# Optimization experiments

Measured on AMD Instinct MI355X. Metric: run time of the kernel, lower is better.

The kernel has to match this reference:

```python
import jax, jax.numpy as jnp
import numpy as np

P = 256          # planes == in_planes
EPS = 1e-5       # BatchNorm eps


def binarize(x):
    # sign with sign(0) -> +1, as in standard binary-net quantizers
    return jnp.where(x >= 0, 1.0, -1.0).astype(x.dtype)


def bin_conv(x, w, stride=1):
    """XNOR-style binarized 3x3 conv: sign(x) * sign(w), scaled by per-out-channel mean |w|."""
    ba = binarize(x)
    bw = binarize(w)
    scale = jnp.mean(jnp.abs(w), axis=(1, 2, 3))  # [O]
    y = jax.lax.conv_general_dilated(
        ba, bw, window_strides=(stride, stride), padding=((1, 1), (1, 1)),
        dimension_numbers=("NCHW", "OIHW", "NCHW"))
    return y * scale[None, :, None, None]


def bn(x, gamma, beta, mean, var):
    # inference-mode BatchNorm2d
    inv = gamma / jnp.sqrt(var + EPS)
    return x * inv[None, :, None, None] + (beta - mean * inv)[None, :, None, None]


def channel_shuffle(x, groups=2):
    b, c, h, w = x.shape
    return x.reshape(b, groups, c // groups, h, w).transpose(0, 2, 1, 3, 4).reshape(b, c, h, w)


def setup_inputs() -> dict:
    key = jax.random.key(0)
    ks = jax.random.split(key, 8)
    B, H, W = 16, 56, 56
    return {
        "x": jax.random.normal(ks[0], (B, 2 * P, H, W), jnp.float32),
        "w1": jax.random.normal(ks[1], (P, P, 3, 3), jnp.float32) * 0.05,
        "w2": jax.random.normal(ks[2], (P, 2 * P, 3, 3), jnp.float32) * 0.05,
        "gamma1": jnp.ones((P,), jnp.float32),
        "beta1": jnp.zeros((P,), jnp.float32),
        "mean1": jax.random.normal(ks[3], (P,), jnp.float32) * 0.1,
        "var1": jax.random.uniform(ks[4], (P,), jnp.float32) + 0.5,
        "gamma2": jnp.ones((P,), jnp.float32),
        "beta2": jnp.zeros((P,), jnp.float32),
        "mean2": jax.random.normal(ks[5], (P,), jnp.float32) * 0.1,
        "var2": jax.random.uniform(ks[6], (P,), jnp.float32) + 0.5,
        "move_bias": jax.random.normal(ks[7], (1, P, 1, 1), jnp.float32) * 0.1,
    }


def reference(x, w1, w2, gamma1, beta1, mean1, var1,
              gamma2, beta2, mean2, var2, move_bias):
    x_act, x_idle = x[:, :P], x[:, P:]
    residual = x_act
    out = bn(bin_conv(x_act, w1, stride=1), gamma1, beta1, mean1, var1)
    out = out + residual
    out = jnp.clip(out, -1.0, 1.0)            # Hardtanh
    x_idle = x_idle + move_bias               # LearnableBias
    out = jnp.concatenate([out, x_idle], axis=1)   # [B, 2P, H, W]
    out = channel_shuffle(out, groups=2)
    residual1 = out[:, :P]
    out = bn(bin_conv(out, w2, stride=1), gamma2, beta2, mean2, var2)
    out = out + residual1
    out = jnp.clip(out, -1.0, 1.0)            # Hardtanh
    return out
```

## Files before the change

### kernel.cpp

```cpp
#include <hip/hip_runtime.h>
#include <cstdint>

typedef unsigned long long u64;

#define HWSZ 3136
#define WD 56
#define NPIX 50176
#define NB 16

__device__ __forceinline__ float clampf(float v){ return fminf(1.0f, fmaxf(-1.0f, v)); }

__global__ __launch_bounds__(256) void k_wprep(
    const float* __restrict__ w1, const float* __restrict__ w2,
    const float* __restrict__ g1, const float* __restrict__ be1,
    const float* __restrict__ m1, const float* __restrict__ v1,
    const float* __restrict__ g2, const float* __restrict__ be2,
    const float* __restrict__ m2, const float* __restrict__ v2,
    u64* __restrict__ w1b, u64* __restrict__ w2e, u64* __restrict__ w2o,
    float* __restrict__ A1, float* __restrict__ B1,
    float* __restrict__ A2, float* __restrict__ B2)
{
    int co  = blockIdx.x;
    int tid = threadIdx.x;
    int wv = tid >> 6, lane = tid & 63;
    int ci = (wv << 6) + lane;

    float s1 = 0.f, s2 = 0.f;
    const float* w1p = w1 + ((size_t)co * 256 + ci) * 9;
#pragma unroll
    for (int t = 0; t < 9; t++) {
        float v = w1p[t];
        s1 += fabsf(v);
        u64 bal = __ballot(v >= 0.f);
        if (lane == 0) w1b[(co * 9 + t) * 4 + wv] = bal;
    }
    const float* wep = w2 + ((size_t)co * 512 + 2 * ci) * 9;
    const float* wop = wep + 9;
#pragma unroll
    for (int t = 0; t < 9; t++) {
        float ve = wep[t], vo = wop[t];
        s2 += fabsf(ve) + fabsf(vo);
        u64 bale = __ballot(ve >= 0.f);
        u64 balo = __ballot(vo >= 0.f);
        if (lane == 0) { w2e[(co * 9 + t) * 4 + wv] = bale; w2o[(co * 9 + t) * 4 + wv] = balo; }
    }
    __shared__ float red1[256], red2[256];
    red1[tid] = s1; red2[tid] = s2;
    __syncthreads();
    for (int off = 128; off > 0; off >>= 1) {
        if (tid < off) { red1[tid] += red1[tid + off]; red2[tid] += red2[tid + off]; }
        __syncthreads();
    }
    if (tid == 0) {
        float scale1 = red1[0] / 2304.f;
        float scale2 = red2[0] / 4608.f;
        float inv1 = g1[co] / sqrtf(v1[co] + 1e-5f);
        float inv2 = g2[co] / sqrtf(v2[co] + 1e-5f);
        A1[co] = scale1 * inv1;  B1[co] = be1[co] - m1[co] * inv1;
        A2[co] = scale2 * inv2;  B2[co] = be2[co] - m2[co] * inv2;
    }
}

__global__ __launch_bounds__(256) void k_pack(
    const float* __restrict__ x, const float* __restrict__ mb,
    u64* __restrict__ bitsA, u64* __restrict__ bitsI)
{
    int tid = threadIdx.x;
    int p = blockIdx.x * 256 + tid;
    int q = blockIdx.y;
    int b = p / HWSZ, hw = p % HWSZ;
    const float* xa = x + ((size_t)(b * 512 + q * 64)) * HWSZ + hw;
    const float* xi = x + ((size_t)(b * 512 + 256 + q * 64)) * HWSZ + hw;
    const float* mbq = mb + q * 64;
    u64 wa = 0, wi = 0;
#pragma unroll 8
    for (int j = 0; j < 64; j++) {
        float va = xa[(size_t)j * HWSZ];
        float vi = xi[(size_t)j * HWSZ] + mbq[j];
        wa |= (u64)(va >= 0.f) << j;
        wi |= (u64)(vi >= 0.f) << j;
    }
    bitsA[(size_t)p * 4 + q] = wa;
    bitsI[(size_t)p * 4 + q] = wi;
}

__global__ __launch_bounds__(256) void k_conv1(
    const float* __restrict__ x, const u64* __restrict__ bitsA,
    const u64* __restrict__ w1b, const float* __restrict__ A1, const float* __restrict__ B1,
    u64* __restrict__ bitsC, float* __restrict__ c1v)
{
    __shared__ u64 sw[2304];
    __shared__ float sA[64], sB[64];
    int tid = threadIdx.x;
    int q = blockIdx.y;
    int cobase = q * 64;
    {
        const u64* src = w1b + (size_t)cobase * 36;
#pragma unroll
        for (int i = 0; i < 9; i++) sw[tid + i * 256] = src[tid + i * 256];
        if (tid < 64) { sA[tid] = A1[cobase + tid]; sB[tid] = B1[cobase + tid]; }
    }
    __syncthreads();

    int p = blockIdx.x * 256 + tid;
    int b = p / HWSZ, hw = p % HWSZ;
    int h = hw / WD, w = hw % WD;

    int acc[64];
#pragma unroll
    for (int i = 0; i < 64; i++) acc[i] = 0;
    int nvalid = 0;
#pragma unroll 1
    for (int t = 0; t < 9; t++) {
        int dy = t / 3 - 1, dx = t % 3 - 1;
        int hh = h + dy, ww = w + dx;
        bool valid = (hh >= 0 && hh < WD && ww >= 0 && ww < WD);
        u64 n0 = 0, n1 = 0, n2 = 0, n3 = 0;
        if (valid) {
            const u64* nb = bitsA + (size_t)(p + dy * WD + dx) * 4;
            n0 = nb[0]; n1 = nb[1]; n2 = nb[2]; n3 = nb[3];
        }
        int mask = valid ? -1 : 0;
        nvalid -= mask;
#pragma unroll
        for (int co = 0; co < 64; co++) {
            const u64* wp = &sw[(co * 9 + t) * 4];
            int pt = __popcll(n0 ^ wp[0]) + __popcll(n1 ^ wp[1])
                   + __popcll(n2 ^ wp[2]) + __popcll(n3 ^ wp[3]);
            acc[co] += pt & mask;
        }
    }
    u64 signw = 0;
    const float* xr = x + ((size_t)(b * 512 + cobase)) * HWSZ + hw;
    float* cv = c1v + (size_t)cobase * NPIX + p;
#pragma unroll
    for (int co = 0; co < 64; co++) {
        int y = (nvalid << 8) - 2 * acc[co];
        float v = (float)y * sA[co] + sB[co] + xr[(size_t)co * HWSZ];
        signw |= (u64)(v >= 0.f) << co;
        if (q < 2) cv[(size_t)co * NPIX] = clampf(v);
    }
    bitsC[(size_t)p * 4 + q] = signw;
}

__global__ __launch_bounds__(256) void k_conv2(
    const float* __restrict__ x, const float* __restrict__ mb,
    const u64* __restrict__ bitsC, const u64* __restrict__ bitsI,
    const u64* __restrict__ w2e, const u64* __restrict__ w2o,
    const float* __restrict__ A2, const float* __restrict__ B2,
    const float* __restrict__ c1v, float* __restrict__ out)
{
    __shared__ u64 se[2304], so[2304];
    __shared__ float sA[64], sB[64], sM[32];
    int tid = threadIdx.x;
    int q = blockIdx.y;
    int cobase = q * 64;
    {
        const u64* srcE = w2e + (size_t)cobase * 36;
        const u64* srcO = w2o + (size_t)cobase * 36;
#pragma unroll
        for (int i = 0; i < 9; i++) { se[tid + i * 256] = srcE[tid + i * 256]; so[tid + i * 256] = srcO[tid + i * 256]; }
        if (tid < 64) { sA[tid] = A2[cobase + tid]; sB[tid] = B2[cobase + tid]; }
        if (tid < 32) { sM[tid] = mb[cobase / 2 + tid]; }
    }
    __syncthreads();

    int p = blockIdx.x * 256 + tid;
    int b = p / HWSZ, hw = p % HWSZ;
    int h = hw / WD, w = hw % WD;

    int acc[64];
#pragma unroll
    for (int i = 0; i < 64; i++) acc[i] = 0;
    int nvalid = 0;
#pragma unroll 1
    for (int t = 0; t < 9; t++) {
        int dy = t / 3 - 1, dx = t % 3 - 1;
        int hh = h + dy, ww = w + dx;
        bool valid = (hh >= 0 && hh < WD && ww >= 0 && ww < WD);
        u64 c0 = 0, c1 = 0, c2 = 0, c3 = 0, i0 = 0, i1 = 0, i2 = 0, i3 = 0;
        if (valid) {
            size_t np = (size_t)(p + dy * WD + dx) * 4;
            c0 = bitsC[np]; c1 = bitsC[np + 1]; c2 = bitsC[np + 2]; c3 = bitsC[np + 3];
            i0 = bitsI[np]; i1 = bitsI[np + 1]; i2 = bitsI[np + 2]; i3 = bitsI[np + 3];
        }
        int mask = valid ? -1 : 0;
        nvalid -= mask;
#pragma unroll
        for (int co = 0; co < 64; co++) {
            const u64* we = &se[(co * 9 + t) * 4];
            const u64* wo = &so[(co * 9 + t) * 4];
            int pt = __popcll(c0 ^ we[0]) + __popcll(c1 ^ we[1])
                   + __popcll(c2 ^ we[2]) + __popcll(c3 ^ we[3])
                   + __popcll(i0 ^ wo[0]) + __popcll(i1 ^ wo[1])
                   + __popcll(i2 ^ wo[2]) + __popcll(i3 ^ wo[3]);
            acc[co] += pt & mask;
        }
    }
    const float* xo = x + ((size_t)(b * 512 + 256 + 32 * q)) * HWSZ + hw;
    const float* cvr = c1v + (size_t)(32 * q) * NPIX + p;
    float* op = out + ((size_t)(b * 256 + cobase)) * HWSZ + hw;
#pragma unroll
    for (int co = 0; co < 64; co++) {
        int y = (nvalid << 9) - 2 * acc[co];
        float v = (float)y * sA[co] + sB[co];
        int cg2 = co >> 1;
        float res;
        if ((co & 1) == 0) res = cvr[(size_t)cg2 * NPIX];
        else               res = xo[(size_t)cg2 * HWSZ] + sM[cg2];
        v += res;
        op[(size_t)co * HWSZ] = clampf(v);
    }
}

extern "C" void kernel_launch(void* const* d_in, const int* in_sizes, int n_in,
                              void* d_out, int out_size, void* d_ws, size_t ws_size,
                              hipStream_t stream)
{
    const float* x   = (const float*)d_in[0];
    const float* w1  = (const float*)d_in[1];
    const float* w2  = (const float*)d_in[2];
    const float* g1  = (const float*)d_in[3];
    const float* be1 = (const float*)d_in[4];
    const float* m1  = (const float*)d_in[5];
    const float* v1  = (const float*)d_in[6];
    const float* g2  = (const float*)d_in[7];
    const float* be2 = (const float*)d_in[8];
    const float* m2  = (const float*)d_in[9];
    const float* v2  = (const float*)d_in[10];
    const float* mb  = (const float*)d_in[11];

    char* ws = (char*)d_ws;
    u64* w1b = (u64*)ws; ws += 73728;
    u64* w2e = (u64*)ws; ws += 73728;
    u64* w2o = (u64*)ws; ws += 73728;
    float* A1 = (float*)ws; ws += 1024;
    float* B1 = (float*)ws; ws += 1024;
    float* A2 = (float*)ws; ws += 1024;
    float* B2 = (float*)ws; ws += 1024;
    u64* bitsA = (u64*)ws; ws += (size_t)NPIX * 4 * 8;
    u64* bitsI = (u64*)ws; ws += (size_t)NPIX * 4 * 8;
    u64* bitsC = (u64*)ws; ws += (size_t)NPIX * 4 * 8;
    float* c1v = (float*)ws; ws += (size_t)128 * NPIX * 4;

    hipLaunchKernelGGL(k_wprep, dim3(256), dim3(256), 0, stream,
                       w1, w2, g1, be1, m1, v1, g2, be2, m2, v2,
                       w1b, w2e, w2o, A1, B1, A2, B2);
    hipLaunchKernelGGL(k_pack, dim3(196, 4), dim3(256), 0, stream, x, mb, bitsA, bitsI);
    hipLaunchKernelGGL(k_conv1, dim3(196, 4), dim3(256), 0, stream,
                       x, bitsA, w1b, A1, B1, bitsC, c1v);
    hipLaunchKernelGGL(k_conv2, dim3(196, 4), dim3(256), 0, stream,
                       x, mb, bitsC, bitsI, w2e, w2o, A2, B2, c1v, (float*)d_out);
}
```

Measured before the change: 462.0 us.

## Restructure binary convs with padded bit layout, per-thread pixel pairs, wave channel groups

The packed activation bits now live in a zero-padded 58x58 layout, so the conv inner loops drop per-tap validity masks. The popcount of padded zero bits is corrected through per-channel border sums precomputed in weight prep. Each thread now computes two adjacent pixels over 16 output channels, with waves splitting the 64-channel group. A row of neighbour bits is loaded once and reused across the three horizontal taps, and weights are read as wave-uniform scalars instead of from LDS in conv1. The intermediate clamp values are stored as bf16 to halve their traffic, and wider vector loads and stores are used. The cost is an extra zeroing kernel, more complex border correction logic, and bf16 rounding of the residual.

Result: slower. 484.1 us (+4.8%).

```diff
diff --git a/kernel.cpp b/kernel.cpp
--- a/kernel.cpp
+++ b/kernel.cpp
@@ -2,13 +2,67 @@
 #include <cstdint>
 
 typedef unsigned long long u64;
+typedef unsigned short u16;
 
 #define HWSZ 3136
 #define WD 56
 #define NPIX 50176
-#define NB 16
+#define HS 58
+#define IMG 3364
 
 __device__ __forceinline__ float clampf(float v){ return fminf(1.0f, fmaxf(-1.0f, v)); }
+__device__ __forceinline__ u16 f2bf(float f){
+    unsigned u = __float_as_uint(f);
+    return (u16)((u + 0x7fffu + ((u >> 16) & 1u)) >> 16);
+}
+__device__ __forceinline__ float bf2f(u16 h){ return __uint_as_float(((unsigned)h) << 16); }
+__device__ __forceinline__ int xp(u64 a, u64 b, int s){
+    u64 x = a ^ b;
+    s += __popc((unsigned)x);
+    s += __popc((unsigned)(x >> 32));
+    return s;
+}
+
+__device__ __forceinline__ void conv_pass(
+    const u64* __restrict__ bits, const u64* __restrict__ wsrc, int colbase,
+    int base, int (&accA)[8][2], int (&accB)[8][2])
+{
+#pragma unroll 1
+    for (int dy = -1; dy <= 1; dy++) {
+        const ulonglong2* rp = (const ulonglong2*)(bits + (size_t)(base + dy * HS) * 4);
+        ulonglong2 plo[4], phi[4];
+#pragma unroll
+        for (int k = 0; k < 4; k++) { plo[k] = rp[2 * k]; phi[k] = rp[2 * k + 1]; }
+        int tb = (dy + 1) * 3;
+#pragma unroll
+        for (int dx = 0; dx < 3; dx++) {
+#pragma unroll
+            for (int co = 0; co < 8; co++) {
+                const u64* wp = wsrc + ((size_t)(colbase + co) * 9 + tb + dx) * 4;
+                u64 wa0 = wp[0], wa1 = wp[1], wb0 = wp[2], wb1 = wp[3];
+#pragma unroll
+                for (int p = 0; p < 2; p++) {
+                    int k = dx + p; int s = accA[co][p];
+                    s = xp(plo[k].x, wa0, s); s = xp(plo[k].y, wa1, s);
+                    s = xp(phi[k].x, wb0, s); s = xp(phi[k].y, wb1, s);
+                    accA[co][p] = s;
+                }
+            }
+#pragma unroll
+            for (int co = 0; co < 8; co++) {
+                const u64* wp = wsrc + ((size_t)(colbase + 8 + co) * 9 + tb + dx) * 4;
+                u64 wa0 = wp[0], wa1 = wp[1], wb0 = wp[2], wb1 = wp[3];
+#pragma unroll
+                for (int p = 0; p < 2; p++) {
+                    int k = dx + p; int s = accB[co][p];
+                    s = xp(plo[k].x, wa0, s); s = xp(plo[k].y, wa1, s);
+                    s = xp(phi[k].x, wb0, s); s = xp(phi[k].y, wb1, s);
+                    accB[co][p] = s;
+                }
+            }
+        }
+    }
+}
 
 __global__ __launch_bounds__(256) void k_wprep(
     const float* __restrict__ w1, const float* __restrict__ w2,
@@ -18,13 +72,16 @@
     const float* __restrict__ m2, const float* __restrict__ v2,
     u64* __restrict__ w1b, u64* __restrict__ w2e, u64* __restrict__ w2o,
     float* __restrict__ A1, float* __restrict__ B1,
-    float* __restrict__ A2, float* __restrict__ B2)
+    float* __restrict__ A2, float* __restrict__ B2,
+    int* __restrict__ C1s, int* __restrict__ C2s)
 {
     int co  = blockIdx.x;
     int tid = threadIdx.x;
     int wv = tid >> 6, lane = tid & 63;
     int ci = (wv << 6) + lane;
 
+    __shared__ int spc1[4][9], spc2[4][9];
+
     float s1 = 0.f, s2 = 0.f;
     const float* w1p = w1 + ((size_t)co * 256 + ci) * 9;
 #pragma unroll
@@ -32,7 +89,7 @@
         float v = w1p[t];
         s1 += fabsf(v);
         u64 bal = __ballot(v >= 0.f);
-        if (lane == 0) w1b[(co * 9 + t) * 4 + wv] = bal;
+        if (lane == 0) { w1b[(co * 9 + t) * 4 + wv] = bal; spc1[wv][t] = __popcll(bal); }
     }
     const float* wep = w2 + ((size_t)co * 512 + 2 * ci) * 9;
     const float* wop = wep + 9;
@@ -42,7 +99,10 @@
         s2 += fabsf(ve) + fabsf(vo);
         u64 bale = __ballot(ve >= 0.f);
         u64 balo = __ballot(vo >= 0.f);
-        if (lane == 0) { w2e[(co * 9 + t) * 4 + wv] = bale; w2o[(co * 9 + t) * 4 + wv] = balo; }
+        if (lane == 0) {
+            w2e[(co * 9 + t) * 4 + wv] = bale; w2o[(co * 9 + t) * 4 + wv] = balo;
+            spc2[wv][t] = __popcll(bale) + __popcll(balo);
+        }
     }
     __shared__ float red1[256], red2[256];
     red1[tid] = s1; red2[tid] = s2;
@@ -58,7 +118,31 @@
         float inv2 = g2[co] / sqrtf(v2[co] + 1e-5f);
         A1[co] = scale1 * inv1;  B1[co] = be1[co] - m1[co] * inv1;
         A2[co] = scale2 * inv2;  B2[co] = be2[co] - m2[co] * inv2;
-    }
+        int pc1[9], pc2[9];
+#pragma unroll
+        for (int t = 0; t < 9; t++) {
+            pc1[t] = spc1[0][t] + spc1[1][t] + spc1[2][t] + spc1[3][t];
+            pc2[t] = spc2[0][t] + spc2[1][t] + spc2[2][t] + spc2[3][t];
+        }
+        int* c1 = C1s + co * 8;
+        c1[0] = pc1[0] + pc1[1] + pc1[2];
+        c1[1] = pc1[6] + pc1[7] + pc1[8];
+        c1[2] = pc1[0] + pc1[3] + pc1[6];
+        c1[3] = pc1[2] + pc1[5] + pc1[8];
+        c1[4] = pc1[0]; c1[5] = pc1[2]; c1[6] = pc1[6]; c1[7] = pc1[8];
+        int* c2 = C2s + co * 8;
+        c2[0] = pc2[0] + pc2[1] + pc2[2];
+        c2[1] = pc2[6] + pc2[7] + pc2[8];
+        c2[2] = pc2[0] + pc2[3] + pc2[6];
+        c2[3] = pc2[2] + pc2[5] + pc2[8];
+        c2[4] = pc2[0]; c2[5] = pc2[2]; c2[6] = pc2[6]; c2[7] = pc2[8];
+    }
+}
+
+__global__ __launch_bounds__(256) void k_zero(ulonglong2* __restrict__ dst, int n)
+{
+    int i = blockIdx.x * 256 + threadIdx.x;
+    if (i < n) { ulonglong2 z; z.x = 0; z.y = 0; dst[i] = z; }
 }
 
 __global__ __launch_bounds__(256) void k_pack(
@@ -69,6 +153,7 @@
     int p = blockIdx.x * 256 + tid;
     int q = blockIdx.y;
     int b = p / HWSZ, hw = p % HWSZ;
+    int h = hw / WD, w = hw % WD;
     const float* xa = x + ((size_t)(b * 512 + q * 64)) * HWSZ + hw;
     const float* xi = x + ((size_t)(b * 512 + 256 + q * 64)) * HWSZ + hw;
     const float* mbq = mb + q * 64;
@@ -80,136 +165,143 @@
         wa |= (u64)(va >= 0.f) << j;
         wi |= (u64)(vi >= 0.f) << j;
     }
-    bitsA[(size_t)p * 4 + q] = wa;
-    bitsI[(size_t)p * 4 + q] = wi;
-}
-
-__global__ __launch_bounds__(256) void k_conv1(
+    size_t pos = ((size_t)b * IMG + (h + 1) * HS + (w + 1)) * 4 + q;
+    bitsA[pos] = wa;
+    bitsI[pos] = wi;
+}
+
+__global__ __launch_bounds__(512, 6) void k_conv1(
     const float* __restrict__ x, const u64* __restrict__ bitsA,
-    const u64* __restrict__ w1b, const float* __restrict__ A1, const float* __restrict__ B1,
-    u64* __restrict__ bitsC, float* __restrict__ c1v)
-{
-    __shared__ u64 sw[2304];
+    const u64* __restrict__ w1b, const float* __restrict__ A1,
+    const float* __restrict__ B1, const int* __restrict__ C1s,
+    u64* __restrict__ bitsC, u16* __restrict__ c1v)
+{
     __shared__ float sA[64], sB[64];
-    int tid = threadIdx.x;
-    int q = blockIdx.y;
-    int cobase = q * 64;
-    {
-        const u64* src = w1b + (size_t)cobase * 36;
-#pragma unroll
-        for (int i = 0; i < 9; i++) sw[tid + i * 256] = src[tid + i * 256];
-        if (tid < 64) { sA[tid] = A1[cobase + tid]; sB[tid] = B1[cobase + tid]; }
-    }
+    __shared__ int scr[512];
+    __shared__ u16 spart[4][256];
+    int tid = threadIdx.x, q = blockIdx.y, cobase = q * 64;
+    if (tid < 64) { sA[tid] = A1[cobase + tid]; sB[tid] = B1[cobase + tid]; }
+    scr[tid] = C1s[cobase * 8 + tid];
     __syncthreads();
 
-    int p = blockIdx.x * 256 + tid;
-    int b = p / HWSZ, hw = p % HWSZ;
-    int h = hw / WD, w = hw % WD;
-
-    int acc[64];
-#pragma unroll
-    for (int i = 0; i < 64; i++) acc[i] = 0;
-    int nvalid = 0;
-#pragma unroll 1
-    for (int t = 0; t < 9; t++) {
-        int dy = t / 3 - 1, dx = t % 3 - 1;
-        int hh = h + dy, ww = w + dx;
-        bool valid = (hh >= 0 && hh < WD && ww >= 0 && ww < WD);
-        u64 n0 = 0, n1 = 0, n2 = 0, n3 = 0;
-        if (valid) {
-            const u64* nb = bitsA + (size_t)(p + dy * WD + dx) * 4;
-            n0 = nb[0]; n1 = nb[1]; n2 = nb[2]; n3 = nb[3];
-        }
-        int mask = valid ? -1 : 0;
-        nvalid -= mask;
-#pragma unroll
-        for (int co = 0; co < 64; co++) {
-            const u64* wp = &sw[(co * 9 + t) * 4];
-            int pt = __popcll(n0 ^ wp[0]) + __popcll(n1 ^ wp[1])
-                   + __popcll(n2 ^ wp[2]) + __popcll(n3 ^ wp[3]);
-            acc[co] += pt & mask;
-        }
-    }
-    u64 signw = 0;
-    const float* xr = x + ((size_t)(b * 512 + cobase)) * HWSZ + hw;
-    float* cv = c1v + (size_t)cobase * NPIX + p;
-#pragma unroll
-    for (int co = 0; co < 64; co++) {
-        int y = (nvalid << 8) - 2 * acc[co];
-        float v = (float)y * sA[co] + sB[co] + xr[(size_t)co * HWSZ];
-        signw |= (u64)(v >= 0.f) << co;
-        if (q < 2) cv[(size_t)co * NPIX] = clampf(v);
-    }
-    bitsC[(size_t)p * 4 + q] = signw;
-}
-
-__global__ __launch_bounds__(256) void k_conv2(
+    int wid = tid >> 6, lane = tid & 63;
+    int gu = __builtin_amdgcn_readfirstlane(wid & 3);
+    int ph = wid >> 2;
+    int pix0 = blockIdx.x * 256 + ph * 128 + lane * 2;
+    int b = pix0 / HWSZ, hw = pix0 % HWSZ, h = hw / WD, w = hw % WD;
+    int base = b * IMG + (h + 1) * HS + w;
+
+    int accA[8][2] = {}, accB[8][2] = {};
+    conv_pass(bitsA, w1b, cobase + (gu << 4), base, accA, accB);
+
+    int mt = (h == 0), mbo = (h == WD - 1);
+    int wl = (w == 0), wr = (w == 54);
+    int nvr = 3 - mt - mbo;
+    int nv0 = nvr * (3 - wl), nv1 = nvr * (3 - wr);
+
+    unsigned sb0 = 0, sb1 = 0;
+    bool wrv = (q < 2);
+#pragma unroll
+    for (int half = 0; half < 2; half++)
+#pragma unroll
+    for (int co = 0; co < 8; co++) {
+        int col = (gu << 4) + half * 8 + co;
+        int coG = cobase + col, bit = half * 8 + co;
+        float A = sA[col], Bc = sB[col];
+        const int* cs = &scr[col * 8];
+        int a0 = half ? accB[co][0] : accA[co][0];
+        int a1 = half ? accB[co][1] : accA[co][1];
+        int ctb = (mt ? cs[0] : 0) + (mbo ? cs[1] : 0);
+        int corr0 = ctb + (wl ? (cs[2] - (mt ? cs[4] : 0) - (mbo ? cs[6] : 0)) : 0);
+        int corr1 = ctb + (wr ? (cs[3] - (mt ? cs[5] : 0) - (mbo ? cs[7] : 0)) : 0);
+        float2 xr = *(const float2*)(x + ((size_t)(b * 512 + coG)) * HWSZ + hw);
+        float v0 = (float)((nv0 << 8) + 2 * (corr0 - a0)) * A + Bc + xr.x;
+        float v1 = (float)((nv1 << 8) + 2 * (corr1 - a1)) * A + Bc + xr.y;
+        sb0 |= (unsigned)(v0 >= 0.f) << bit;
+        sb1 |= (unsigned)(v1 >= 0.f) << bit;
+        if (wrv) {
+            ushort2 st; st.x = f2bf(clampf(v0)); st.y = f2bf(clampf(v1));
+            *(ushort2*)(c1v + (size_t)coG * NPIX + pix0) = st;
+        }
+    }
+    spart[gu][ph * 128 + lane * 2]     = (u16)sb0;
+    spart[gu][ph * 128 + lane * 2 + 1] = (u16)sb1;
+    __syncthreads();
+    if ((wid & 3) == 0) {
+#pragma unroll
+        for (int p = 0; p < 2; p++) {
+            int pi = ph * 128 + lane * 2 + p;
+            u64 word = (u64)spart[0][pi] | ((u64)spart[1][pi] << 16)
+                     | ((u64)spart[2][pi] << 32) | ((u64)spart[3][pi] << 48);
+            bitsC[(size_t)(base + 1 + p) * 4 + q] = word;
+        }
+    }
+}
+
+__global__ __launch_bounds__(512, 6) void k_conv2(
     const float* __restrict__ x, const float* __restrict__ mb,
     const u64* __restrict__ bitsC, const u64* __restrict__ bitsI,
     const u64* __restrict__ w2e, const u64* __restrict__ w2o,
     const float* __restrict__ A2, const float* __restrict__ B2,
-    const float* __restrict__ c1v, float* __restrict__ out)
-{
-    __shared__ u64 se[2304], so[2304];
+    const int* __restrict__ C2s,
+    const u16* __restrict__ c1v, float* __restrict__ out)
+{
+    __shared__ __align__(16) u64 se[2304], so[2304];
     __shared__ float sA[64], sB[64], sM[32];
-    int tid = threadIdx.x;
-    int q = blockIdx.y;
-    int cobase = q * 64;
+    __shared__ int scr[512];
+    int tid = threadIdx.x, q = blockIdx.y, cobase = q * 64;
     {
         const u64* srcE = w2e + (size_t)cobase * 36;
         const u64* srcO = w2o + (size_t)cobase * 36;
-#pragma unroll
-        for (int i = 0; i < 9; i++) { se[tid + i * 256] = srcE[tid + i * 256]; so[tid + i * 256] = srcO[tid + i * 256]; }
+        for (int i = tid; i < 2304; i += 512) { se[i] = srcE[i]; so[i] = srcO[i]; }
         if (tid < 64) { sA[tid] = A2[cobase + tid]; sB[tid] = B2[cobase + tid]; }
-        if (tid < 32) { sM[tid] = mb[cobase / 2 + tid]; }
+        if (tid >= 64 && tid < 96) sM[tid - 64] = mb[q * 32 + tid - 64];
+        scr[tid] = C2s[cobase * 8 + tid];
     }
     __syncthreads();
 
-    int p = blockIdx.x * 256 + tid;
-    int b = p / HWSZ, hw = p % HWSZ;
-    int h = hw / WD, w = hw % WD;
-
-    int acc[64];
-#pragma unroll
-    for (int i = 0; i < 64; i++) acc[i] = 0;
-    int nvalid = 0;
-#pragma unroll 1
-    for (int t = 0; t < 9; t++) {
-        int dy = t / 3 - 1, dx = t % 3 - 1;
-        int hh = h + dy, ww = w + dx;
-        bool valid = (hh >= 0 && hh < WD && ww >= 0 && ww < WD);
-        u64 c0 = 0, c1 = 0, c2 = 0, c3 = 0, i0 = 0, i1 = 0, i2 = 0, i3 = 0;
-        if (valid) {
-            size_t np = (size_t)(p + dy * WD + dx) * 4;
-            c0 = bitsC[np]; c1 = bitsC[np + 1]; c2 = bitsC[np + 2]; c3 = bitsC[np + 3];
-            i0 = bitsI[np]; i1 = bitsI[np + 1]; i2 = bitsI[np + 2]; i3 = bitsI[np + 3];
-        }
-        int mask = valid ? -1 : 0;
-        nvalid -= mask;
-#pragma unroll
-        for (int co = 0; co < 64; co++) {
-            const u64* we = &se[(co * 9 + t) * 4];
-            const u64* wo = &so[(co * 9 + t) * 4];
-            int pt = __popcll(c0 ^ we[0]) + __popcll(c1 ^ we[1])
-                   + __popcll(c2 ^ we[2]) + __popcll(c3 ^ we[3])
-                   + __popcll(i0 ^ wo[0]) + __popcll(i1 ^ wo[1])
-                   + __popcll(i2 ^ wo[2]) + __popcll(i3 ^ wo[3]);
-            acc[co] += pt & mask;
-        }
-    }
-    const float* xo = x + ((size_t)(b * 512 + 256 + 32 * q)) * HWSZ + hw;
-    const float* cvr = c1v + (size_t)(32 * q) * NPIX + p;
-    float* op = out + ((size_t)(b * 256 + cobase)) * HWSZ + hw;
-#pragma unroll
-    for (int co = 0; co < 64; co++) {
-        int y = (nvalid << 9) - 2 * acc[co];
-        float v = (float)y * sA[co] + sB[co];
-        int cg2 = co >> 1;
-        float res;
-        if ((co & 1) == 0) res = cvr[(size_t)cg2 * NPIX];
-        else               res = xo[(size_t)cg2 * HWSZ] + sM[cg2];
-        v += res;
-        op[(size_t)co * HWSZ] = clampf(v);
+    int wid = tid >> 6, lane = tid & 63;
+    int gu = __builtin_amdgcn_readfirstlane(wid & 3);
+    int ph = wid >> 2;
+    int pix0 = blockIdx.x * 256 + ph * 128 + lane * 2;
+    int b = pix0 / HWSZ, hw = pix0 % HWSZ, h = hw / WD, w = hw % WD;
+    int base = b * IMG + (h + 1) * HS + w;
+
+    int accA[8][2] = {}, accB[8][2] = {};
+    conv_pass(bitsC, se, gu << 4, base, accA, accB);
+    conv_pass(bitsI, so, gu << 4, base, accA, accB);
+
+    int mt = (h == 0), mbo = (h == WD - 1);
+    int wl = (w == 0), wr = (w == 54);
+    int nvr = 3 - mt - mbo;
+    int nv0 = nvr * (3 - wl), nv1 = nvr * (3 - wr);
+
+#pragma unroll
+    for (int half = 0; half < 2; half++)
+#pragma unroll
+    for (int co = 0; co < 8; co++) {
+        int col = (gu << 4) + half * 8 + co;
+        int coG = cobase + col, cg2 = coG >> 1;
+        float A = sA[col], Bc = sB[col];
+        const int* cs = &scr[col * 8];
+        int a0 = half ? accB[co][0] : accA[co][0];
+        int a1 = half ? accB[co][1] : accA[co][1];
+        int ctb = (mt ? cs[0] : 0) + (mbo ? cs[1] : 0);
+        int corr0 = ctb + (wl ? (cs[2] - (mt ? cs[4] : 0) - (mbo ? cs[6] : 0)) : 0);
+        int corr1 = ctb + (wr ? (cs[3] - (mt ? cs[5] : 0) - (mbo ? cs[7] : 0)) : 0);
+        float r0, r1;
+        if ((co & 1) == 0) {
+            ushort2 cv = *(const ushort2*)(c1v + (size_t)cg2 * NPIX + pix0);
+            r0 = bf2f(cv.x); r1 = bf2f(cv.y);
+        } else {
+            float2 xi = *(const float2*)(x + ((size_t)(b * 512 + 256 + cg2)) * HWSZ + hw);
+            float mv = sM[col >> 1];
+            r0 = xi.x + mv; r1 = xi.y + mv;
+        }
+        float2 ov;
+        ov.x = clampf((float)((nv0 << 9) + 2 * (corr0 - a0)) * A + Bc + r0);
+        ov.y = clampf((float)((nv1 << 9) + 2 * (corr1 - a1)) * A + Bc + r1);
+        *(float2*)(out + ((size_t)(b * 256 + coG)) * HWSZ + hw) = ov;
     }
 }
 
@@ -238,17 +330,23 @@
     float* B1 = (float*)ws; ws += 1024;
     float* A2 = (float*)ws; ws += 1024;
     float* B2 = (float*)ws; ws += 1024;
-    u64* bitsA = (u64*)ws; ws += (size_t)NPIX * 4 * 8;
-    u64* bitsI = (u64*)ws; ws += (size_t)NPIX * 4 * 8;
-    u64* bitsC = (u64*)ws; ws += (size_t)NPIX * 4 * 8;
-    float* c1v = (float*)ws; ws += (size_t)128 * NPIX * 4;
+    int* C1s = (int*)ws; ws += 8192;
+    int* C2s = (int*)ws; ws += 8192;
+    u64* bitsA = (u64*)ws; ws += (size_t)16 * IMG * 4 * 8;
+    u64* bitsI = (u64*)ws; ws += (size_t)16 * IMG * 4 * 8;
+    u64* bitsC = (u64*)ws; ws += (size_t)16 * IMG * 4 * 8;
+    u16* c1v = (u16*)ws; ws += (size_t)128 * NPIX * 2;
+
+    int nzero2 = (int)(3 * (size_t)16 * IMG * 4 * 8 / 16);
 
     hipLaunchKernelGGL(k_wprep, dim3(256), dim3(256), 0, stream,
                        w1, w2, g1, be1, m1, v1, g2, be2, m2, v2,
-                       w1b, w2e, w2o, A1, B1, A2, B2);
+                       w1b, w2e, w2o, A1, B1, A2, B2, C1s, C2s);
+    hipLaunchKernelGGL(k_zero, dim3((nzero2 + 255) / 256), dim3(256), 0, stream,
+                       (ulonglong2*)bitsA, nzero2);
     hipLaunchKernelGGL(k_pack, dim3(196, 4), dim3(256), 0, stream, x, mb, bitsA, bitsI);
-    hipLaunchKernelGGL(k_conv1, dim3(196, 4), dim3(256), 0, stream,
-                       x, bitsA, w1b, A1, B1, bitsC, c1v);
-    hipLaunchKernelGGL(k_conv2, dim3(196, 4), dim3(256), 0, stream,
-                       x, mb, bitsC, bitsI, w2e, w2o, A2, B2, c1v, (float*)d_out);
-}
+    hipLaunchKernelGGL(k_conv1, dim3(196, 4), dim3(512), 0, stream,
+                       x, bitsA, w1b, A1, B1, C1s, bitsC, c1v);
+    hipLaunchKernelGGL(k_conv2, dim3(196, 4), dim3(512), 0, stream,
+                       x, mb, bitsC, bitsI, w2e, w2o, A2, B2, C2s, c1v, (float*)d_out);
+}
```
